# Performance work log

Measured on AMD Instinct MI355X. Metric: run time of the kernel, lower is better.

## Reference

```python
import jax, jax.numpy as jnp
import numpy as np

B, N, C, K = 8, 49104, 90, 1000  # batch, anchors, classes, pre-NMS top-k cap
NEG = -1e9


def _decode(reg, anc):
    # anchors ltrb -> cxcywh, apply reg, back to ltrb (matches decode_boxes)
    l, t, r, b = anc[..., 0], anc[..., 1], anc[..., 2], anc[..., 3]
    w_a, h_a = r - l, b - t
    cx_a, cy_a = l + w_a / 2, t + h_a / 2
    cx = cx_a + reg[..., 0] * w_a
    cy = cy_a + reg[..., 1] * h_a
    w = w_a * jnp.exp(reg[..., 2])
    h = h_a * jnp.exp(reg[..., 3])
    left, top = cx - w / 2, cy - h / 2
    return jnp.stack([left, top, left + w, top + h], -1)


def _iou(boxes):  # [K,4] -> [K,K]
    area = (boxes[:, 2] - boxes[:, 0]) * (boxes[:, 3] - boxes[:, 1])
    lt = jnp.maximum(boxes[:, None, :2], boxes[None, :, :2])
    rb = jnp.minimum(boxes[:, None, 2:], boxes[None, :, 2:])
    wh = jnp.clip(rb - lt, 0.0)
    inter = wh[..., 0] * wh[..., 1]
    return inter / (area[:, None] + area[None, :] - inter + 1e-9)


def _per_image(cls, reg, anchors, size, size_ori, score_thresh, nms_thresh):
    scores = jnp.max(cls, axis=-1)                       # [N]
    labels = jnp.argmax(cls, axis=-1).astype(jnp.int32)  # [N]
    valid = scores >= score_thresh
    boxes = _decode(reg, anchors)                        # [N,4] ltrb
    H = size[0].astype(jnp.float32)
    W = size[1].astype(jnp.float32)
    x = jnp.clip(boxes[..., 0::2], 0.0, W - 1.0)
    y = jnp.clip(boxes[..., 1::2], 0.0, H - 1.0)
    boxes = jnp.stack([x[..., 0], y[..., 0], x[..., 1], y[..., 1]], -1)
    # fixed-size substitute for nonzero(): take top-K by masked score
    ms = jnp.where(valid, scores, NEG)
    top_s, idx = jax.lax.top_k(ms, K)
    b, l, v = boxes[idx], labels[idx], valid[idx]        # [K,4],[K],[K]
    # batched_nms trick: offset boxes per class so classes never overlap
    off = l.astype(jnp.float32) * (jnp.maximum(W, H) + 1.0)
    iou = _iou(b + off[:, None])                         # [K,K]
    ar = jnp.arange(K)
    def body(i, supp):
        keep_i = v[i] & jnp.logical_not(supp[i])
        return supp | (keep_i & (iou[i] > nms_thresh) & (ar > i))
    supp = jax.lax.fori_loop(0, K, body, jnp.zeros((K,), bool))
    keep = v & jnp.logical_not(supp)
    scale = size_ori[0].astype(jnp.float32) / H
    b = b * scale
    out5 = jnp.concatenate(
        [jnp.where(keep[:, None], b, 0.0), jnp.where(keep, top_s, 0.0)[:, None]], -1)
    return out5, jnp.where(keep, l, -1), keep


def setup_inputs() -> dict:
    key = jax.random.key(0)
    k1, k2, k3, k4, k5, k6 = jax.random.split(key, 6)
    classifications = jax.random.uniform(k1, (B, N, C), dtype=jnp.float32)
    regressions = jax.random.normal(k2, (B, N, 4), dtype=jnp.float32) * 0.1
    cx = jax.random.uniform(k3, (N,), minval=0.0, maxval=512.0)
    cy = jax.random.uniform(k4, (N,), minval=0.0, maxval=512.0)
    w = jax.random.uniform(k5, (N,), minval=16.0, maxval=256.0)
    h = jax.random.uniform(k6, (N,), minval=16.0, maxval=256.0)
    anchors = jnp.stack([cx - w / 2, cy - h / 2, cx + w / 2, cy + h / 2], -1)
    return {
        'classifications': classifications,
        'regressions': regressions,
        'anchors': anchors,
        'image_sizes': jnp.full((B, 2), 512, dtype=jnp.int32),
        'image_sizes_ori': jnp.full((B, 2), 768, dtype=jnp.int32),
        'score_thresh': jnp.float32(0.999),
        'nms_thresh': jnp.float32(0.5),
    }


def reference(classifications, regressions, anchors, image_sizes, image_sizes_ori, score_thresh, nms_thresh):
    out5, labels, keep = jax.vmap(
        _per_image, in_axes=(0, 0, None, 0, 0, None, None))(
        classifications, regressions, anchors, image_sizes, image_sizes_ori,
        score_thresh, nms_thresh)
    return out5, labels, keep
```

## Files before the change

### kernel.cpp

```cpp
#include <hip/hip_runtime.h>
#include <stdint.h>

#define NB 8
#define NN 49104
#define NNP 49152
#define NC 90
#define NK 1000
#define KW 16
#define CAP2 8192
#define SEG 1024
#define CHUNK 6144
#define NB2 4352
#define NB2P 5120

typedef unsigned long long u64;

__global__ void k_score(const float* __restrict__ cls,
                        const float* __restrict__ thr_p,
                        u64* __restrict__ keys) {
  __shared__ float lds[64 * NC];
  int b = blockIdx.y;
  int t0 = blockIdx.x * 64;
  int acnt = NN - t0; if (acnt > 64) acnt = 64;
  const float4* src = (const float4*)(cls + ((size_t)b * NN + t0) * NC);
  float4* dst = (float4*)lds;
  int elems4 = acnt * NC / 4;
  for (int t = threadIdx.x; t < elems4; t += 256) dst[t] = src[t];
  __syncthreads();
  int a = threadIdx.x >> 2, q = threadIdx.x & 3;
  float best = -1e30f; int bc = 0;
  if (a < acnt) {
    for (int c = q; c < NC; c += 4) {
      float v = lds[a * NC + c];
      if (v > best) { best = v; bc = c; }
    }
    float ov; int oc;
    ov = __shfl_xor(best, 1); oc = __shfl_xor(bc, 1);
    if (ov > best || (ov == best && oc < bc)) { best = ov; bc = oc; }
    ov = __shfl_xor(best, 2); oc = __shfl_xor(bc, 2);
    if (ov > best || (ov == best && oc < bc)) { best = ov; bc = oc; }
  }
  if (q == 0) {
    unsigned idx = (unsigned)(t0 + a);
    u64 key = 0ULL;
    if (a < acnt && best >= *thr_p)
      key = ((u64)__float_as_uint(best) << 32) |
            ((u64)(0xFFFFu - idx) << 16) | (u64)(unsigned)bc;
    keys[(size_t)b * NNP + idx] = key;
  }
}

__global__ __launch_bounds__(1024) void k_compact(const u64* __restrict__ keys,
                                                  u64* __restrict__ ckeys,
                                                  unsigned* __restrict__ segcnt) {
  __shared__ unsigned scnt;
  int tid = threadIdx.x;
  int lane = tid & 63;
  int b = blockIdx.y, chunk = blockIdx.x;
  if (tid == 0) scnt = 0u;
  __syncthreads();
  const u64* src = keys + (size_t)b * NNP + (size_t)chunk * CHUNK;
  u64* dst = ckeys + (size_t)b * CAP2 + (size_t)chunk * SEG;
  u64 k0 = src[tid], k1 = src[tid + 1024], k2 = src[tid + 2048];
  u64 k3 = src[tid + 3072], k4 = src[tid + 4096], k5 = src[tid + 5120];
  u64 lmask = (1ULL << lane) - 1ULL;
  u64 kk[6] = {k0, k1, k2, k3, k4, k5};
#pragma unroll
  for (int j = 0; j < 6; j++) {
    u64 key = kk[j];
    bool valid = key != 0ULL;
    u64 m = __ballot(valid);
    if (m) {
      int leader = (int)__ffsll((unsigned long long)m) - 1;
      unsigned base = 0;
      if (lane == leader) base = atomicAdd(&scnt, (unsigned)__popcll(m));
      base = __shfl(base, leader);
      if (valid) {
        unsigned pos = base + (unsigned)__popcll(m & lmask);
        if (pos < SEG) dst[pos] = key;
      }
    }
  }
  __syncthreads();
  if (tid == 0) {
    unsigned total = scnt; if (total > SEG) total = SEG;
    segcnt[b * 8 + chunk] = total;
  }
}

__device__ __forceinline__ void decode_box(const float4 rg, const float4 an,
                                           float W, float H, float* out) {
#pragma clang fp contract(off)
  float l = an.x, t = an.y, r = an.z, bo = an.w;
  float wa = r - l, ha = bo - t;
  float cxa = l + wa * 0.5f, cya = t + ha * 0.5f;
  float cx = cxa + rg.x * wa;
  float cy = cya + rg.y * ha;
  float w = wa * expf(rg.z);
  float h = ha * expf(rg.w);
  float left = cx - w * 0.5f, top = cy - h * 0.5f;
  float right = left + w, botm = top + h;
  out[0] = fminf(fmaxf(left, 0.f), W - 1.f);
  out[1] = fminf(fmaxf(top, 0.f), H - 1.f);
  out[2] = fminf(fmaxf(right, 0.f), W - 1.f);
  out[3] = fminf(fmaxf(botm, 0.f), H - 1.f);
}

__global__ __launch_bounds__(1024) void k_sortnms(
    const u64* __restrict__ ckeys, const unsigned* __restrict__ segcnt,
    const float* __restrict__ regs, const float* __restrict__ anch,
    const int* __restrict__ isz, const int* __restrict__ iszo,
    const float* __restrict__ nthr_p, float* __restrict__ out) {
#pragma clang fp contract(off)
  __shared__ __align__(16) char S[151552];
  __shared__ unsigned wsum[16];
  __shared__ unsigned sofs[9];
  __shared__ int lcnt[NC + 1];
  __shared__ int lofs[NC + 1];
  __shared__ int lcur[NC];
  __shared__ u64 nzv[16];
  __shared__ u64 skeep[KW];

  u64* cand = (u64*)S;
  u64* outk = (u64*)(S + 65536);
  unsigned* hist = (unsigned*)(S + 131072);

  int tid = threadIdx.x;
  int lane = tid & 63, wid = tid >> 6;
  int b = blockIdx.x;

  for (int i = tid; i < NB2P; i += 1024) hist[i] = 0u;
  if (tid == 0) {
    unsigned acc = 0;
    for (int s = 0; s < 8; s++) {
      unsigned c = segcnt[b * 8 + s]; if (c > SEG) c = SEG;
      sofs[s] = acc; acc += c;
    }
    sofs[8] = acc;
  }
  __syncthreads();
  unsigned total = sofs[8];

  for (int s = 0; s < 8; s++) {
    unsigned o = sofs[s], c = sofs[s + 1] - o;
    const u64* srcp = ckeys + (size_t)b * CAP2 + (size_t)s * SEG;
    for (unsigned i = tid; i < c; i += 1024) cand[o + i] = srcp[i];
  }
  __syncthreads();

  for (unsigned p = tid; p < total; p += 1024) {
    unsigned bin = (0x3F800000u - (unsigned)(cand[p] >> 32) - 1u) >> 2;
    if (bin >= NB2) bin = NB2 - 1;
    atomicAdd(&hist[bin], 1u);
  }
  __syncthreads();

  int base5 = tid * 5;
  unsigned mysum = 0;
#pragma unroll
  for (int i = 0; i < 5; i++) mysum += hist[base5 + i];
  unsigned v = mysum;
  for (int d = 1; d < 64; d <<= 1) {
    unsigned o = __shfl_up(v, d);
    if (lane >= d) v += o;
  }
  if (lane == 63) wsum[wid] = v;
  __syncthreads();
  if (tid == 0) {
    unsigned acc = 0;
    for (int w2 = 0; w2 < 16; w2++) { unsigned c = wsum[w2]; wsum[w2] = acc; acc += c; }
  }
  __syncthreads();
  unsigned running = wsum[wid] + v - mysum;
#pragma unroll
  for (int i = 0; i < 5; i++) {
    unsigned c = hist[base5 + i];
    hist[base5 + i] = running;
    running += c;
  }
  __syncthreads();

  for (unsigned p = tid; p < total; p += 1024) {
    u64 key = cand[p];
    unsigned bin = (0x3F800000u - (unsigned)(key >> 32) - 1u) >> 2;
    if (bin >= NB2) bin = NB2 - 1;
    unsigned pos = atomicAdd(&hist[bin], 1u);
    if (pos < CAP2) outk[pos] = key;
  }
  __syncthreads();

  for (int bin = tid; bin < NB2; bin += 1024) {
    unsigned hi = hist[bin];
    unsigned lo = bin ? hist[bin - 1] : 0u;
    if (hi > CAP2) hi = CAP2;
    if (lo > CAP2) lo = CAP2;
    if (hi > lo + 1) {
      for (unsigned i2 = lo + 1; i2 < hi; i2++) {
        u64 kx = outk[i2];
        int j = (int)i2 - 1;
        while (j >= (int)lo && outk[j] < kx) { outk[j + 1] = outk[j]; j--; }
        outk[j + 1] = kx;
      }
    }
  }
  __syncthreads();

  int n = (int)total; if (n > NK) n = NK;
  float4* bo = (float4*)S;
  unsigned short* llab = (unsigned short*)(S + 16000);
  unsigned short* sidx = (unsigned short*)(S + 18000);
  unsigned short* send = (unsigned short*)(S + 20000);
  u64* sm = (u64*)(S + 22016);

  float H = (float)isz[b * 2 + 0];
  float W = (float)isz[b * 2 + 1];
  float scale = (float)iszo[b * 2 + 0] / H;
  float offmul = fmaxf(W, H) + 1.0f;
  for (int k = tid; k < n; k += 1024) {
    u64 key = outk[k];
    float sc = __uint_as_float((unsigned)(key >> 32));
    unsigned idx = 0xFFFFu - (unsigned)((key >> 16) & 0xFFFFull);
    int lab = (int)(key & 0xFFFFull);
    float raw[4];
    float4 rg = ((const float4*)regs)[(size_t)b * NN + idx];
    float4 an = ((const float4*)anch)[idx];
    decode_box(rg, an, W, H, raw);
    float off = (float)lab * offmul;
    bo[k] = make_float4(raw[0] + off, raw[1] + off, raw[2] + off, raw[3] + off);
    llab[k] = (unsigned short)lab;
    int g = b * NK + k;
    float* o5 = out + (size_t)g * 5;
    o5[0] = raw[0] * scale; o5[1] = raw[1] * scale;
    o5[2] = raw[2] * scale; o5[3] = raw[3] * scale;
    o5[4] = sc;
    out[(size_t)NB * NK * 5 + g] = (float)lab;
  }
  __syncthreads();

  for (int t = tid; t < NK * KW; t += 1024) sm[t] = 0ULL;
  if (tid < 16) nzv[tid] = 0ULL;
  if (tid <= NC) lcnt[tid] = 0;
  __syncthreads();

  for (int k = tid; k < n; k += 1024) atomicAdd(&lcnt[(int)llab[k]], 1);
  __syncthreads();
  if (tid == 0) {
    int acc = 0;
    for (int c = 0; c < NC; c++) { lofs[c] = acc; acc += lcnt[c]; }
    lofs[NC] = acc;
  }
  __syncthreads();
  if (tid < NC) lcur[tid] = lofs[tid];
  __syncthreads();
  for (int k = tid; k < n; k += 1024) {
    int lab = (int)llab[k];
    int pos = atomicAdd(&lcur[lab], 1);
    sidx[pos] = (unsigned short)k;
    send[pos] = (unsigned short)lofs[lab + 1];
  }
  __syncthreads();

  float thr = *nthr_p;
  for (int p = tid; p < n; p += 1024) {
    int e = (int)send[p];
    int a = (int)sidx[p];
    for (int q2 = p + 1; q2 < e; q2++) {
      int c2 = (int)sidx[q2];
      int i = a < c2 ? a : c2;
      int j = a < c2 ? c2 : a;
      float4 Bb = bo[i];
      float4 Cc = bo[j];
      float x0 = Bb.x, y0 = Bb.y, x1 = Bb.z, y1 = Bb.w;
      float ai = (x1 - x0) * (y1 - y0);
      float aj = (Cc.z - Cc.x) * (Cc.w - Cc.y);
      float ltx = fmaxf(x0, Cc.x), lty = fmaxf(y0, Cc.y);
      float rbx = fminf(x1, Cc.z), rby = fminf(y1, Cc.w);
      float ww = fmaxf(rbx - ltx, 0.f), hh = fmaxf(rby - lty, 0.f);
      float inter = ww * hh;
      float den = ((ai + aj) - inter) + 1e-9f;
      float iou = inter / den;
      if (iou > thr) {
        atomicOr(&sm[(size_t)i * KW + (j >> 6)], 1ULL << (j & 63));
        atomicOr(&nzv[i >> 6], 1ULL << (i & 63));
      }
    }
  }
  __syncthreads();

  if (tid < 16) {
    int base = tid * 64;
    u64 validw;
    if (n <= base) validw = 0ULL;
    else if (n >= base + 64) validw = ~0ULL;
    else validw = (~0ULL) >> (64 - (n - base));
    nzv[tid] &= validw;
  }
  __syncthreads();

  int ml = tid & 15;
  if (tid < 64) {
    int bb2 = ml * 64;
    u64 rem;
    if (n <= bb2) rem = ~0ULL;
    else if (n >= bb2 + 64) rem = 0ULL;
    else rem = (~0ULL) << (n - bb2);
    for (int w = 0; w < 16; w++) {
      unsigned rl = (unsigned)__builtin_amdgcn_readlane((int)(unsigned)rem, w);
      unsigned rh = (unsigned)__builtin_amdgcn_readlane((int)(unsigned)(rem >> 32), w);
      u64 rw = ((u64)rh << 32) | (u64)rl;
      u64 active = nzv[w] & ~rw;
      while (active) {
        int i = (int)__ffsll((unsigned long long)active) - 1;
        active &= active - 1ULL;
        u64 crow = sm[(size_t)(w * 64 + i) * KW + ml];
        rem |= crow;
        unsigned cl = (unsigned)__builtin_amdgcn_readlane((int)(unsigned)crow, w);
        unsigned ch = (unsigned)__builtin_amdgcn_readlane((int)(unsigned)(crow >> 32), w);
        rw |= ((u64)ch << 32) | (u64)cl;
        active &= ~rw;
      }
      if (lane == 0) skeep[w] = ~rw;
    }
  }
  __syncthreads();

  for (int k = tid; k < NK; k += 1024) {
    int g = b * NK + k;
    int keep = (int)((skeep[k >> 6] >> (k & 63)) & 1ULL);
    if (keep) {
      out[(size_t)NB * NK * 6 + g] = 1.0f;
    } else {
      float* o5 = out + (size_t)g * 5;
      o5[0] = 0.f; o5[1] = 0.f; o5[2] = 0.f; o5[3] = 0.f; o5[4] = 0.f;
      out[(size_t)NB * NK * 5 + g] = -1.0f;
      out[(size_t)NB * NK * 6 + g] = 0.0f;
    }
  }
}

extern "C" void kernel_launch(void* const* d_in, const int* in_sizes, int n_in,
                              void* d_out, int out_size, void* d_ws, size_t ws_size,
                              hipStream_t stream) {
  const float* cls = (const float*)d_in[0];
  const float* regs = (const float*)d_in[1];
  const float* anch = (const float*)d_in[2];
  const int* isz = (const int*)d_in[3];
  const int* iszo = (const int*)d_in[4];
  const float* sthr = (const float*)d_in[5];
  const float* nthr = (const float*)d_in[6];
  float* out = (float*)d_out;

  char* p = (char*)d_ws;
  auto alloc = [&](size_t bytes) {
    char* r = p;
    p += (bytes + 255) & ~(size_t)255;
    return r;
  };
  u64* keys = (u64*)alloc((size_t)NB * NNP * 8);
  u64* ckeys = (u64*)alloc((size_t)NB * CAP2 * 8);
  unsigned* segcnt = (unsigned*)alloc((size_t)NB * 8 * 4);

  hipLaunchKernelGGL(k_score, dim3(NNP / 64, NB), dim3(256), 0, stream,
                     cls, sthr, keys);
  hipLaunchKernelGGL(k_compact, dim3(8, NB), dim3(1024), 0, stream,
                     keys, ckeys, segcnt);
  hipLaunchKernelGGL(k_sortnms, dim3(NB), dim3(1024), 0, stream,
                     ckeys, segcnt, regs, anch, isz, iszo, nthr, out);
}
```

Baseline: 57.71 us.

## Fuse score, compact and sort-NMS into one persistent kernel with per-image completion counters

Merges the three launches into a single kernel. The first 8 blocks are NMS workers that spin on a per-image atomic counter until all score blocks for that image have published their keys. The remaining blocks do the max/argmax scoring over 256 anchors each. The separate compaction pass is folded into the worker, which reads all keys, compacts them with ballot and atomics, and builds the histogram in the same loop. This removes launch gaps and an intermediate buffer. It adds a memset launch, relies on the worker blocks being resident while score blocks run, and makes each worker scan all 49k keys serially with one block.

```diff
diff --git a/kernel.cpp b/kernel.cpp
--- a/kernel.cpp
+++ b/kernel.cpp
@@ -8,85 +8,13 @@
 #define NK 1000
 #define KW 16
 #define CAP2 8192
-#define SEG 1024
-#define CHUNK 6144
 #define NB2 4352
 #define NB2P 5120
+#define SBLK 192
+#define SANCH 256
+#define NWORK 8
 
 typedef unsigned long long u64;
-
-__global__ void k_score(const float* __restrict__ cls,
-                        const float* __restrict__ thr_p,
-                        u64* __restrict__ keys) {
-  __shared__ float lds[64 * NC];
-  int b = blockIdx.y;
-  int t0 = blockIdx.x * 64;
-  int acnt = NN - t0; if (acnt > 64) acnt = 64;
-  const float4* src = (const float4*)(cls + ((size_t)b * NN + t0) * NC);
-  float4* dst = (float4*)lds;
-  int elems4 = acnt * NC / 4;
-  for (int t = threadIdx.x; t < elems4; t += 256) dst[t] = src[t];
-  __syncthreads();
-  int a = threadIdx.x >> 2, q = threadIdx.x & 3;
-  float best = -1e30f; int bc = 0;
-  if (a < acnt) {
-    for (int c = q; c < NC; c += 4) {
-      float v = lds[a * NC + c];
-      if (v > best) { best = v; bc = c; }
-    }
-    float ov; int oc;
-    ov = __shfl_xor(best, 1); oc = __shfl_xor(bc, 1);
-    if (ov > best || (ov == best && oc < bc)) { best = ov; bc = oc; }
-    ov = __shfl_xor(best, 2); oc = __shfl_xor(bc, 2);
-    if (ov > best || (ov == best && oc < bc)) { best = ov; bc = oc; }
-  }
-  if (q == 0) {
-    unsigned idx = (unsigned)(t0 + a);
-    u64 key = 0ULL;
-    if (a < acnt && best >= *thr_p)
-      key = ((u64)__float_as_uint(best) << 32) |
-            ((u64)(0xFFFFu - idx) << 16) | (u64)(unsigned)bc;
-    keys[(size_t)b * NNP + idx] = key;
-  }
-}
-
-__global__ __launch_bounds__(1024) void k_compact(const u64* __restrict__ keys,
-                                                  u64* __restrict__ ckeys,
-                                                  unsigned* __restrict__ segcnt) {
-  __shared__ unsigned scnt;
-  int tid = threadIdx.x;
-  int lane = tid & 63;
-  int b = blockIdx.y, chunk = blockIdx.x;
-  if (tid == 0) scnt = 0u;
-  __syncthreads();
-  const u64* src = keys + (size_t)b * NNP + (size_t)chunk * CHUNK;
-  u64* dst = ckeys + (size_t)b * CAP2 + (size_t)chunk * SEG;
-  u64 k0 = src[tid], k1 = src[tid + 1024], k2 = src[tid + 2048];
-  u64 k3 = src[tid + 3072], k4 = src[tid + 4096], k5 = src[tid + 5120];
-  u64 lmask = (1ULL << lane) - 1ULL;
-  u64 kk[6] = {k0, k1, k2, k3, k4, k5};
-#pragma unroll
-  for (int j = 0; j < 6; j++) {
-    u64 key = kk[j];
-    bool valid = key != 0ULL;
-    u64 m = __ballot(valid);
-    if (m) {
-      int leader = (int)__ffsll((unsigned long long)m) - 1;
-      unsigned base = 0;
-      if (lane == leader) base = atomicAdd(&scnt, (unsigned)__popcll(m));
-      base = __shfl(base, leader);
-      if (valid) {
-        unsigned pos = base + (unsigned)__popcll(m & lmask);
-        if (pos < SEG) dst[pos] = key;
-      }
-    }
-  }
-  __syncthreads();
-  if (tid == 0) {
-    unsigned total = scnt; if (total > SEG) total = SEG;
-    segcnt[b * 8 + chunk] = total;
-  }
-}
 
 __device__ __forceinline__ void decode_box(const float4 rg, const float4 an,
                                            float W, float H, float* out) {
@@ -106,54 +34,113 @@
   out[3] = fminf(fmaxf(botm, 0.f), H - 1.f);
 }
 
-__global__ __launch_bounds__(1024) void k_sortnms(
-    const u64* __restrict__ ckeys, const unsigned* __restrict__ segcnt,
-    const float* __restrict__ regs, const float* __restrict__ anch,
-    const int* __restrict__ isz, const int* __restrict__ iszo,
-    const float* __restrict__ nthr_p, float* __restrict__ out) {
+__global__ __launch_bounds__(1024) void k_mega(
+    const float* __restrict__ cls, const float* __restrict__ regs,
+    const float* __restrict__ anch, const int* __restrict__ isz,
+    const int* __restrict__ iszo, const float* __restrict__ sthr_p,
+    const float* __restrict__ nthr_p, u64* __restrict__ keys,
+    unsigned* __restrict__ score_done, float* __restrict__ out) {
 #pragma clang fp contract(off)
   __shared__ __align__(16) char S[151552];
   __shared__ unsigned wsum[16];
-  __shared__ unsigned sofs[9];
   __shared__ int lcnt[NC + 1];
   __shared__ int lofs[NC + 1];
   __shared__ int lcur[NC];
   __shared__ u64 nzv[16];
   __shared__ u64 skeep[KW];
-
+  __shared__ unsigned scnt;
+
+  int tid = threadIdx.x;
+  int bid = blockIdx.x;
+
+  if (bid >= NWORK) {
+    int sbid = bid - NWORK;
+    int b = sbid / SBLK, blk = sbid % SBLK;
+    int t0 = blk * SANCH;
+    float* lds = (float*)S;
+    int acnt = NN - t0; if (acnt > SANCH) acnt = SANCH;
+    const float4* src = (const float4*)(cls + ((size_t)b * NN + t0) * NC);
+    float4* dst = (float4*)lds;
+    int elems4 = acnt * NC / 4;
+    for (int t = tid; t < elems4; t += 1024) dst[t] = src[t];
+    __syncthreads();
+    int a = tid >> 2, q = tid & 3;
+    float best = -1e30f; int bc = 0;
+    if (a < acnt) {
+      for (int c = q; c < NC; c += 4) {
+        float v = lds[a * NC + c];
+        if (v > best) { best = v; bc = c; }
+      }
+      float ov; int oc;
+      ov = __shfl_xor(best, 1); oc = __shfl_xor(bc, 1);
+      if (ov > best || (ov == best && oc < bc)) { best = ov; bc = oc; }
+      ov = __shfl_xor(best, 2); oc = __shfl_xor(bc, 2);
+      if (ov > best || (ov == best && oc < bc)) { best = ov; bc = oc; }
+    }
+    if (q == 0) {
+      unsigned idx = (unsigned)(t0 + a);
+      u64 key = 0ULL;
+      if (a < acnt && best >= *sthr_p)
+        key = ((u64)__float_as_uint(best) << 32) |
+              ((u64)(0xFFFFu - idx) << 16) | (u64)(unsigned)bc;
+      keys[(size_t)b * NNP + idx] = key;
+    }
+    __syncthreads();
+    if (tid == 0) {
+      __threadfence();
+      __hip_atomic_fetch_add(&score_done[b], 1u, __ATOMIC_RELEASE,
+                             __HIP_MEMORY_SCOPE_AGENT);
+    }
+    return;
+  }
+
+  int b = bid;
   u64* cand = (u64*)S;
   u64* outk = (u64*)(S + 65536);
   unsigned* hist = (unsigned*)(S + 131072);
-
-  int tid = threadIdx.x;
   int lane = tid & 63, wid = tid >> 6;
-  int b = blockIdx.x;
 
   for (int i = tid; i < NB2P; i += 1024) hist[i] = 0u;
+  if (tid == 0) scnt = 0u;
+  __syncthreads();
+
   if (tid == 0) {
-    unsigned acc = 0;
-    for (int s = 0; s < 8; s++) {
-      unsigned c = segcnt[b * 8 + s]; if (c > SEG) c = SEG;
-      sofs[s] = acc; acc += c;
-    }
-    sofs[8] = acc;
-  }
-  __syncthreads();
-  unsigned total = sofs[8];
-
-  for (int s = 0; s < 8; s++) {
-    unsigned o = sofs[s], c = sofs[s + 1] - o;
-    const u64* srcp = ckeys + (size_t)b * CAP2 + (size_t)s * SEG;
-    for (unsigned i = tid; i < c; i += 1024) cand[o + i] = srcp[i];
-  }
-  __syncthreads();
-
-  for (unsigned p = tid; p < total; p += 1024) {
-    unsigned bin = (0x3F800000u - (unsigned)(cand[p] >> 32) - 1u) >> 2;
-    if (bin >= NB2) bin = NB2 - 1;
-    atomicAdd(&hist[bin], 1u);
-  }
-  __syncthreads();
+    while (__hip_atomic_load(&score_done[b], __ATOMIC_ACQUIRE,
+                             __HIP_MEMORY_SCOPE_AGENT) < SBLK)
+      __builtin_amdgcn_s_sleep(2);
+  }
+  __syncthreads();
+
+  {
+    const u64* srcp = keys + (size_t)b * NNP;
+    u64 lmask = (1ULL << lane) - 1ULL;
+    for (int base = 0; base < 48; base += 8) {
+      u64 kk[8];
+#pragma unroll
+      for (int j = 0; j < 8; j++) kk[j] = srcp[(base + j) * 1024 + tid];
+#pragma unroll
+      for (int j = 0; j < 8; j++) {
+        u64 key = kk[j];
+        bool valid = key != 0ULL;
+        u64 m = __ballot(valid);
+        if (m) {
+          int leader = (int)__ffsll((unsigned long long)m) - 1;
+          unsigned bpos = 0;
+          if (lane == leader) bpos = atomicAdd(&scnt, (unsigned)__popcll(m));
+          bpos = __shfl(bpos, leader);
+          if (valid) {
+            unsigned pos = bpos + (unsigned)__popcll(m & lmask);
+            if (pos < CAP2) cand[pos] = key;
+            unsigned bin = (0x3F800000u - (unsigned)(key >> 32) - 1u) >> 2;
+            if (bin >= NB2) bin = NB2 - 1;
+            atomicAdd(&hist[bin], 1u);
+          }
+        }
+      }
+    }
+  }
+  __syncthreads();
+  unsigned total = scnt; if (total > CAP2) total = CAP2;
 
   int base5 = tid * 5;
   unsigned mysum = 0;
@@ -357,13 +344,10 @@
     return r;
   };
   u64* keys = (u64*)alloc((size_t)NB * NNP * 8);
-  u64* ckeys = (u64*)alloc((size_t)NB * CAP2 * 8);
-  unsigned* segcnt = (unsigned*)alloc((size_t)NB * 8 * 4);
-
-  hipLaunchKernelGGL(k_score, dim3(NNP / 64, NB), dim3(256), 0, stream,
-                     cls, sthr, keys);
-  hipLaunchKernelGGL(k_compact, dim3(8, NB), dim3(1024), 0, stream,
-                     keys, ckeys, segcnt);
-  hipLaunchKernelGGL(k_sortnms, dim3(NB), dim3(1024), 0, stream,
-                     ckeys, segcnt, regs, anch, isz, iszo, nthr, out);
+  unsigned* score_done = (unsigned*)alloc((size_t)NB * 4);
+
+  hipMemsetAsync(score_done, 0, (size_t)NB * sizeof(unsigned), stream);
+  hipLaunchKernelGGL(k_mega, dim3(NWORK + NB * SBLK), dim3(1024), 0, stream,
+                     cls, regs, anch, isz, iszo, sthr, nthr,
+                     keys, score_done, out);
 }
```

Result: slower. 124.1 us (+115.1%).
